# Kernel tuning notes

Hardware: AMD Instinct MI355X
Metric: run time of the kernel (lower is better)

Reference implementation:

```python
import jax, jax.numpy as jnp
import numpy as np

B, T, C, H = 8, 1024, 768, 12
HD = C // H  # 64


def setup_inputs() -> dict:
    key = jax.random.key(0)
    ks = jax.random.split(key, 9)
    s = 0.02
    x = jax.random.normal(ks[0], (B, T, C), dtype=jnp.float32)
    mask = jnp.tril(jnp.ones((T, T), dtype=bool))[None, None, :, :]  # causal [1,1,T,T]
    wq = jax.random.normal(ks[1], (C, C), dtype=jnp.float32) * s
    wk = jax.random.normal(ks[2], (C, C), dtype=jnp.float32) * s
    wv = jax.random.normal(ks[3], (C, C), dtype=jnp.float32) * s
    wo = jax.random.normal(ks[4], (C, C), dtype=jnp.float32) * s
    bq = jnp.zeros((C,), dtype=jnp.float32)
    bk = jnp.zeros((C,), dtype=jnp.float32)
    bv = jnp.zeros((C,), dtype=jnp.float32)
    bo = jnp.zeros((C,), dtype=jnp.float32)
    return {"x": x, "mask": mask, "wq": wq, "bq": bq, "wk": wk, "bk": bk,
            "wv": wv, "bv": bv, "wo": wo, "bo": bo}


def reference(x, mask, wq, bq, wk, bk, wv, bv, wo, bo):
    Bx, Tx, Cx = x.shape
    # QKV projections (flax Dense: y = x @ W + b)
    q = (x @ wq + bq).reshape(Bx, Tx, H, HD).transpose(0, 2, 1, 3)  # [B,H,T,hd]
    k = (x @ wk + bk).reshape(Bx, Tx, H, HD).transpose(0, 2, 1, 3)
    v = (x @ wv + bv).reshape(Bx, Tx, H, HD).transpose(0, 2, 1, 3)
    attn = jnp.einsum('bhtd,bhsd->bhts', q, k) / jnp.sqrt(jnp.float32(HD))
    attn = jnp.where(mask, attn, jnp.float32(-1e9))
    attn = jax.nn.softmax(attn, axis=-1)
    out = jnp.einsum('bhts,bhsd->bhtd', attn, v)  # [B,H,T,hd]
    out = out.transpose(0, 2, 1, 3).reshape(Bx, Tx, Cx)
    return out @ wo + bo
```

## Files before the change

kernel.cpp:

```cpp
#include <hip/hip_runtime.h>
#include <hip/hip_bf16.h>

typedef __bf16 bf16_t;
typedef __bf16 bf16x8 __attribute__((ext_vector_type(8)));
typedef float f32x4 __attribute__((ext_vector_type(4)));

#define NB 8
#define NT 1024
#define NC 768
#define NH 12
#define NHD 64

__device__ __forceinline__ f32x4 mfma16(bf16x8 a, bf16x8 b, f32x4 c) {
  return __builtin_amdgcn_mfma_f32_16x16x32_bf16(a, b, c, 0, 0, 0);
}

__device__ __forceinline__ void gld_lds16(const void* g, void* l) {
  __builtin_amdgcn_global_load_lds((const __attribute__((address_space(1))) void*)g,
                                   (__attribute__((address_space(3))) void*)l, 16, 0, 0);
}

__global__ void cvt_x(const float* __restrict__ in, bf16_t* __restrict__ out, int n4) {
  int i = blockIdx.x * blockDim.x + threadIdx.x;
  if (i >= n4) return;
  float4 v = ((const float4*)in)[i];
  bf16_t o[4] = {(bf16_t)v.x, (bf16_t)v.y, (bf16_t)v.z, (bf16_t)v.w};
  *(uint2*)(out + i * 4) = *(uint2*)o;
}

__global__ void transpose_w(const float* __restrict__ wq, const float* __restrict__ wk,
                            const float* __restrict__ wv, const float* __restrict__ wo,
                            bf16_t* __restrict__ wqkvT, bf16_t* __restrict__ woT) {
  __shared__ float tile[32][33];
  const int m = blockIdx.z;
  const float* in = (m == 0) ? wq : (m == 1) ? wk : (m == 2) ? wv : wo;
  bf16_t* out = (m == 3) ? woT : (wqkvT + m * NC * NC);
  const int tx = threadIdx.x & 31, ty = threadIdx.x >> 5;
  const int x = blockIdx.x * 32 + tx;
  const int y0 = blockIdx.y * 32;
#pragma unroll
  for (int i = 0; i < 32; i += 8)
    tile[ty + i][tx] = in[(size_t)(y0 + ty + i) * NC + x];
  __syncthreads();
  const int ox = y0 + tx;
  const int oy0 = blockIdx.x * 32;
#pragma unroll
  for (int i = 0; i < 32; i += 8)
    out[(size_t)(oy0 + ty + i) * NC + ox] = (bf16_t)tile[tx][ty + i];
}

template <int MODE>
__global__ __launch_bounds__(256) void gemm128(
    const bf16_t* __restrict__ A, const bf16_t* __restrict__ BT, int K,
    const float* __restrict__ b0, const float* __restrict__ b1,
    const float* __restrict__ b2, float* __restrict__ outF,
    bf16_t* __restrict__ out0, bf16_t* __restrict__ out1,
    bf16_t* __restrict__ out2) {
  __shared__ __align__(16) bf16_t lA[128 * 32];
  __shared__ __align__(16) bf16_t lB[128 * 32];
  const int tid = threadIdx.x;
  const int lane = tid & 63, wave = tid >> 6;
  const int quad = lane >> 4, l16 = lane & 15;
  const int bm = blockIdx.x * 128, bn = blockIdx.y * 128;
  const int wr = wave >> 1, wc = wave & 1;

  const int ra = tid >> 2;
  const int cc = tid & 3;
  const int kca = cc ^ ((ra >> 1) & 3);

  f32x4 acc[4][4] = {};
  char* lAb = (char*)lA;
  char* lBb = (char*)lB;

  for (int k0 = 0; k0 < K; k0 += 32) {
    __syncthreads();
    gld_lds16(A + (size_t)(bm + ra) * K + k0 + kca * 8, lAb + wave * 1024);
    gld_lds16(A + (size_t)(bm + 64 + ra) * K + k0 + kca * 8, lAb + 4096 + wave * 1024);
    gld_lds16(BT + (size_t)(bn + ra) * K + k0 + kca * 8, lBb + wave * 1024);
    gld_lds16(BT + (size_t)(bn + 64 + ra) * K + k0 + kca * 8, lBb + 4096 + wave * 1024);
    __syncthreads();

    bf16x8 af[4], bfr[4];
#pragma unroll
    for (int i = 0; i < 4; i++) {
      int row = wr * 64 + i * 16 + l16;
      int ch = quad ^ ((row >> 1) & 3);
      af[i] = *(const bf16x8*)(lAb + row * 64 + ch * 16);
    }
#pragma unroll
    for (int j = 0; j < 4; j++) {
      int row = wc * 64 + j * 16 + l16;
      int ch = quad ^ ((row >> 1) & 3);
      bfr[j] = *(const bf16x8*)(lBb + row * 64 + ch * 16);
    }
#pragma unroll
    for (int i = 0; i < 4; i++)
#pragma unroll
      for (int j = 0; j < 4; j++)
        acc[i][j] = mfma16(af[i], bfr[j], acc[i][j]);
  }

  if (MODE == 0) {
#pragma unroll
    for (int j = 0; j < 4; j++) {
      int n = bn + wc * 64 + j * 16 + l16;
      float bias = b0[n];
#pragma unroll
      for (int i = 0; i < 4; i++) {
        int m0 = bm + wr * 64 + i * 16 + quad * 4;
#pragma unroll
        for (int r = 0; r < 4; r++)
          outF[(size_t)(m0 + r) * NC + n] = acc[i][j][r] + bias;
      }
    }
  } else {
#pragma unroll
    for (int j = 0; j < 4; j++) {
      int n = bn + wc * 64 + j * 16 + l16;
      int sel = n / 768;
      int nl = n - sel * 768;
      int h = nl >> 6, d = nl & 63;
      const float* bp = (sel == 0) ? b0 : (sel == 1) ? b1 : b2;
      bf16_t* dst = (sel == 0) ? out0 : (sel == 1) ? out1 : out2;
      float bias = bp[nl];
#pragma unroll
      for (int i = 0; i < 4; i++) {
        int m0 = bm + wr * 64 + i * 16 + quad * 4;
#pragma unroll
        for (int r = 0; r < 4; r++) {
          int m = m0 + r;
          int bb = m >> 10, t = m & 1023;
          float v = acc[i][j][r] + bias;
          if (sel < 2)
            dst[((size_t)(bb * NH + h) * NT + t) * NHD + d] = (bf16_t)v;
          else
            dst[((size_t)(bb * NH + h) * NHD + d) * NT + t] = (bf16_t)v;
        }
      }
    }
  }
}

__global__ __launch_bounds__(256) void attn_fwd(
    const bf16_t* __restrict__ Q, const bf16_t* __restrict__ Kt,
    const bf16_t* __restrict__ VT, bf16_t* __restrict__ AO) {
  __shared__ __align__(16) bf16_t lK[64 * 72];
  __shared__ __align__(16) bf16_t lV[64 * 72];
  __shared__ __align__(16) bf16_t lP[8][16 * 72];
  const int tid = threadIdx.x, lane = tid & 63, wave = tid >> 6;
  const int quad = lane >> 4, l16 = lane & 15;
  const int bx = blockIdx.x;
  const int bh = blockIdx.y;
  const int b = bh / NH, h = bh - b * NH;
  const int qtA = bx, qtB = 15 - bx;
  const int jmax = qtB;

  const size_t qbase = (size_t)bh * NT;
  const size_t qoffA = (qbase + qtA * 64 + wave * 16 + l16) * NHD;
  const size_t qoffB = (qbase + qtB * 64 + wave * 16 + l16) * NHD;
  const bf16x8 aqA0 = *(const bf16x8*)(Q + qoffA + quad * 8);
  const bf16x8 aqA1 = *(const bf16x8*)(Q + qoffA + 32 + quad * 8);
  const bf16x8 aqB0 = *(const bf16x8*)(Q + qoffB + quad * 8);
  const bf16x8 aqB1 = *(const bf16x8*)(Q + qoffB + 32 + quad * 8);

  f32x4 mA = {-1e30f, -1e30f, -1e30f, -1e30f}, mB = mA;
  f32x4 lA_ = {0.f, 0.f, 0.f, 0.f}, lB_ = lA_;
  f32x4 OfA[4] = {}, OfB[4] = {};

  const int r0 = tid >> 3, p0 = tid & 7;
  const bf16_t* Kg0 = Kt + qbase * NHD;
  const bf16_t* Vg0 = VT + (size_t)bh * 64 * NT;

  uint4 gk0 = *(const uint4*)(Kg0 + (size_t)r0 * 64 + p0 * 8);
  uint4 gk1 = *(const uint4*)(Kg0 + (size_t)(r0 + 32) * 64 + p0 * 8);
  uint4 gv0 = *(const uint4*)(Vg0 + (size_t)r0 * NT + p0 * 8);
  uint4 gv1 = *(const uint4*)(Vg0 + (size_t)(r0 + 32) * NT + p0 * 8);

  bf16_t* lPA = lP[wave * 2 + 0];
  bf16_t* lPB = lP[wave * 2 + 1];
  const int sb = quad ^ (l16 >> 2);

  for (int j = 0; j <= jmax; ++j) {
    __syncthreads();
    *(uint4*)(lK + r0 * 72 + p0 * 8) = gk0;
    *(uint4*)(lK + (r0 + 32) * 72 + p0 * 8) = gk1;
    *(uint4*)(lV + r0 * 72 + p0 * 8) = gv0;
    *(uint4*)(lV + (r0 + 32) * 72 + p0 * 8) = gv1;
    __syncthreads();
    if (j < jmax) {
      const bf16_t* Kg = Kg0 + (size_t)(j + 1) * 64 * NHD;
      const bf16_t* Vg = Vg0 + (j + 1) * 64;
      gk0 = *(const uint4*)(Kg + (size_t)r0 * 64 + p0 * 8);
      gk1 = *(const uint4*)(Kg + (size_t)(r0 + 32) * 64 + p0 * 8);
      gv0 = *(const uint4*)(Vg + (size_t)r0 * NT + p0 * 8);
      gv1 = *(const uint4*)(Vg + (size_t)(r0 + 32) * NT + p0 * 8);
    }
    const bool actA = (j <= qtA);

#pragma unroll
    for (int g = 0; g < 2; g++) {
      if (g == 0 && !actA) continue;
      const bf16x8 q0 = g ? aqB0 : aqA0;
      const bf16x8 q1 = g ? aqB1 : aqA1;
      f32x4* Of = g ? OfB : OfA;
      f32x4& mrun = g ? mB : mA;
      f32x4& lrun = g ? lB_ : lA_;
      const bool diag = g ? (j == qtB) : (j == qtA);

      f32x4 s[4] = {};
#pragma unroll
      for (int nn = 0; nn < 4; nn++) {
        int row = nn * 16 + l16;
        bf16x8 k0 = *(const bf16x8*)(lK + row * 72 + quad * 8);
        bf16x8 k1 = *(const bf16x8*)(lK + row * 72 + 32 + quad * 8);
        s[nn] = mfma16(q0, k0, s[nn]);
        s[nn] = mfma16(q1, k1, s[nn]);
      }
#pragma unroll
      for (int nn = 0; nn < 4; nn++) s[nn] *= 0.125f;

      if (diag) {
#pragma unroll
        for (int nn = 0; nn < 4; nn++) {
          int key = nn * 16 + l16;
#pragma unroll
          for (int r = 0; r < 4; r++) {
            int qrow = wave * 16 + quad * 4 + r;
            if (key > qrow) s[nn][r] = -1e30f;
          }
        }
      }

      f32x4 mx = s[0];
#pragma unroll
      for (int nn = 1; nn < 4; nn++)
#pragma unroll
        for (int r = 0; r < 4; r++) mx[r] = fmaxf(mx[r], s[nn][r]);
#pragma unroll
      for (int off = 8; off >= 1; off >>= 1)
#pragma unroll
        for (int r = 0; r < 4; r++) mx[r] = fmaxf(mx[r], __shfl_xor(mx[r], off, 64));

      f32x4 mnew, alpha;
#pragma unroll
      for (int r = 0; r < 4; r++) {
        mnew[r] = fmaxf(mrun[r], mx[r]);
        alpha[r] = __expf(mrun[r] - mnew[r]);
        mrun[r] = mnew[r];
      }
      f32x4 rs = {0.f, 0.f, 0.f, 0.f};
#pragma unroll
      for (int nn = 0; nn < 4; nn++)
#pragma unroll
        for (int r = 0; r < 4; r++) {
          float pv = __expf(s[nn][r] - mnew[r]);
          s[nn][r] = pv;
          rs[r] += pv;
        }
#pragma unroll
      for (int off = 8; off >= 1; off >>= 1)
#pragma unroll
        for (int r = 0; r < 4; r++) rs[r] += __shfl_xor(rs[r], off, 64);
#pragma unroll
      for (int r = 0; r < 4; r++) lrun[r] = lrun[r] * alpha[r] + rs[r];
#pragma unroll
      for (int dd = 0; dd < 4; dd++)
#pragma unroll
        for (int r = 0; r < 4; r++) Of[dd][r] *= alpha[r];

      bf16_t* lPw = g ? lPB : lPA;
#pragma unroll
      for (int nn = 0; nn < 4; nn++)
#pragma unroll
        for (int r = 0; r < 4; r++)
          lPw[(quad * 4 + r) * 72 + ((nn * 16 + l16) ^ (quad * 8))] = (bf16_t)s[nn][r];
    }
    __syncthreads();

#pragma unroll
    for (int g = 0; g < 2; g++) {
      if (g == 0 && !actA) continue;
      f32x4* Of = g ? OfB : OfA;
      bf16_t* lPw = g ? lPB : lPA;
      const bf16x8 ap0 = *(const bf16x8*)(lPw + l16 * 72 + sb * 8);
      const bf16x8 ap1 = *(const bf16x8*)(lPw + l16 * 72 + (sb + 4) * 8);
#pragma unroll
      for (int dd = 0; dd < 4; dd++) {
        int row = dd * 16 + l16;
        bf16x8 v0 = *(const bf16x8*)(lV + row * 72 + quad * 8);
        bf16x8 v1 = *(const bf16x8*)(lV + row * 72 + 32 + quad * 8);
        Of[dd] = mfma16(ap0, v0, Of[dd]);
        Of[dd] = mfma16(ap1, v1, Of[dd]);
      }
    }
  }

#pragma unroll
  for (int g = 0; g < 2; g++) {
    f32x4* Of = g ? OfB : OfA;
    f32x4& lrun = g ? lB_ : lA_;
    const int qt = g ? qtB : qtA;
    f32x4 inv;
#pragma unroll
    for (int r = 0; r < 4; r++) inv[r] = 1.0f / lrun[r];
    const int tq = qt * 64 + wave * 16 + quad * 4;
#pragma unroll
    for (int dd = 0; dd < 4; dd++) {
      int col = h * 64 + dd * 16 + l16;
#pragma unroll
      for (int r = 0; r < 4; r++)
        AO[((size_t)b * NT + tq + r) * NC + col] = (bf16_t)(Of[dd][r] * inv[r]);
    }
  }
}

extern "C" void kernel_launch(void* const* d_in, const int* in_sizes, int n_in,
                              void* d_out, int out_size, void* d_ws, size_t ws_size,
                              hipStream_t stream) {
  const float* x = (const float*)d_in[0];
  const float* wq = (const float*)d_in[2];
  const float* bq = (const float*)d_in[3];
  const float* wk = (const float*)d_in[4];
  const float* bk = (const float*)d_in[5];
  const float* wv = (const float*)d_in[6];
  const float* bv = (const float*)d_in[7];
  const float* wo = (const float*)d_in[8];
  const float* bo = (const float*)d_in[9];

  float* outF = (float*)d_out;
  bf16_t* Qb = (bf16_t*)d_out;
  bf16_t* ws = (bf16_t*)d_ws;
  bf16_t* xb = ws;
  bf16_t* wqkvT = xb + (size_t)NB * NT * NC;
  bf16_t* woT = wqkvT + (size_t)2304 * 768;
  bf16_t* Kb = woT + (size_t)768 * 768;
  bf16_t* VTb = Kb + (size_t)NB * NH * NT * NHD;
  bf16_t* AO = VTb + (size_t)NB * NH * NT * NHD;

  const int n4 = NB * NT * NC / 4;
  cvt_x<<<(n4 + 255) / 256, 256, 0, stream>>>(x, xb, n4);
  transpose_w<<<dim3(24, 24, 4), 256, 0, stream>>>(wq, wk, wv, wo, wqkvT, woT);
  gemm128<1><<<dim3(64, 18), 256, 0, stream>>>(xb, wqkvT, NC, bq, bk, bv,
                                               nullptr, Qb, Kb, VTb);
  attn_fwd<<<dim3(8, 96), 256, 0, stream>>>(Qb, Kb, VTb, AO);
  gemm128<0><<<dim3(64, 6), 256, 0, stream>>>(AO, woT, NC, bo, nullptr, nullptr,
                                              outF, nullptr, nullptr, nullptr);
}
```

Before: 241.4 us.

## Transpose V in a separate kernel, fold softmax scale into Q, retile output GEMM

The QKV GEMM now writes V in the same row-major head layout as Q and K, which replaces the strided transposed stores in its epilogue. A new LDS-tiled kernel then produces the transposed V layout the attention kernel expects. The 1/sqrt(d) scale is applied to Q in the projection epilogue, so the per-tile multiply in attention goes away. In attention, a block-wide barrier before the P·V step becomes a per-wave LDS waitcnt, since each wave reads only its own P buffer. The output projection uses 64-row tiles, giving twice as many blocks. The costs are an extra kernel launch and an extra pass over V, and the barrier removal relies on per-wave ownership of the P buffers.

New measurement: 233.8 us. -3.1%, faster.

```diff
diff --git a/kernel.cpp b/kernel.cpp
--- a/kernel.cpp
+++ b/kernel.cpp
@@ -49,65 +49,85 @@
     out[(size_t)(oy0 + ty + i) * NC + ox] = (bf16_t)tile[tx][ty + i];
 }
 
-template <int MODE>
-__global__ __launch_bounds__(256) void gemm128(
+__global__ void transpose_v(const bf16_t* __restrict__ V, bf16_t* __restrict__ VT) {
+  __shared__ bf16_t tile[32][33];
+  const int bh = blockIdx.z;
+  const int x0 = blockIdx.x * 32;
+  const int y0 = blockIdx.y * 32;
+  const int tx = threadIdx.x & 31, ty = threadIdx.x >> 5;
+  const bf16_t* in = V + (size_t)bh * NT * NHD;
+  bf16_t* out = VT + (size_t)bh * NHD * NT;
+#pragma unroll
+  for (int i = 0; i < 32; i += 8)
+    tile[ty + i][tx] = in[(size_t)(y0 + ty + i) * NHD + x0 + tx];
+  __syncthreads();
+#pragma unroll
+  for (int i = 0; i < 32; i += 8)
+    out[(size_t)(x0 + ty + i) * NT + y0 + tx] = tile[tx][ty + i];
+}
+
+template <int MODE, int BM>
+__global__ __launch_bounds__(256) void gemm_t(
     const bf16_t* __restrict__ A, const bf16_t* __restrict__ BT, int K,
     const float* __restrict__ b0, const float* __restrict__ b1,
     const float* __restrict__ b2, float* __restrict__ outF,
     bf16_t* __restrict__ out0, bf16_t* __restrict__ out1,
     bf16_t* __restrict__ out2) {
-  __shared__ __align__(16) bf16_t lA[128 * 32];
+  constexpr int NJ = (BM == 128) ? 4 : 2;
+  __shared__ __align__(16) bf16_t lA[BM * 32];
   __shared__ __align__(16) bf16_t lB[128 * 32];
   const int tid = threadIdx.x;
   const int lane = tid & 63, wave = tid >> 6;
   const int quad = lane >> 4, l16 = lane & 15;
-  const int bm = blockIdx.x * 128, bn = blockIdx.y * 128;
-  const int wr = wave >> 1, wc = wave & 1;
+  const int bm = blockIdx.x * BM, bn = blockIdx.y * 128;
+  const int wm = (BM == 128) ? (wave >> 1) * 64 : 0;
+  const int wn = (BM == 128) ? (wave & 1) * 64 : wave * 32;
 
   const int ra = tid >> 2;
   const int cc = tid & 3;
   const int kca = cc ^ ((ra >> 1) & 3);
 
-  f32x4 acc[4][4] = {};
+  f32x4 acc[4][NJ] = {};
   char* lAb = (char*)lA;
   char* lBb = (char*)lB;
 
   for (int k0 = 0; k0 < K; k0 += 32) {
     __syncthreads();
     gld_lds16(A + (size_t)(bm + ra) * K + k0 + kca * 8, lAb + wave * 1024);
-    gld_lds16(A + (size_t)(bm + 64 + ra) * K + k0 + kca * 8, lAb + 4096 + wave * 1024);
+    if (BM == 128)
+      gld_lds16(A + (size_t)(bm + 64 + ra) * K + k0 + kca * 8, lAb + 4096 + wave * 1024);
     gld_lds16(BT + (size_t)(bn + ra) * K + k0 + kca * 8, lBb + wave * 1024);
     gld_lds16(BT + (size_t)(bn + 64 + ra) * K + k0 + kca * 8, lBb + 4096 + wave * 1024);
     __syncthreads();
 
-    bf16x8 af[4], bfr[4];
+    bf16x8 af[4], bfr[NJ];
 #pragma unroll
     for (int i = 0; i < 4; i++) {
-      int row = wr * 64 + i * 16 + l16;
+      int row = wm + i * 16 + l16;
       int ch = quad ^ ((row >> 1) & 3);
       af[i] = *(const bf16x8*)(lAb + row * 64 + ch * 16);
     }
 #pragma unroll
-    for (int j = 0; j < 4; j++) {
-      int row = wc * 64 + j * 16 + l16;
+    for (int j = 0; j < NJ; j++) {
+      int row = wn + j * 16 + l16;
       int ch = quad ^ ((row >> 1) & 3);
       bfr[j] = *(const bf16x8*)(lBb + row * 64 + ch * 16);
     }
 #pragma unroll
     for (int i = 0; i < 4; i++)
 #pragma unroll
-      for (int j = 0; j < 4; j++)
+      for (int j = 0; j < NJ; j++)
         acc[i][j] = mfma16(af[i], bfr[j], acc[i][j]);
   }
 
   if (MODE == 0) {
 #pragma unroll
-    for (int j = 0; j < 4; j++) {
-      int n = bn + wc * 64 + j * 16 + l16;
+    for (int j = 0; j < NJ; j++) {
+      int n = bn + wn + j * 16 + l16;
       float bias = b0[n];
 #pragma unroll
       for (int i = 0; i < 4; i++) {
-        int m0 = bm + wr * 64 + i * 16 + quad * 4;
+        int m0 = bm + wm + i * 16 + quad * 4;
 #pragma unroll
         for (int r = 0; r < 4; r++)
           outF[(size_t)(m0 + r) * NC + n] = acc[i][j][r] + bias;
@@ -115,26 +135,24 @@
     }
   } else {
 #pragma unroll
-    for (int j = 0; j < 4; j++) {
-      int n = bn + wc * 64 + j * 16 + l16;
+    for (int j = 0; j < NJ; j++) {
+      int n = bn + wn + j * 16 + l16;
       int sel = n / 768;
       int nl = n - sel * 768;
       int h = nl >> 6, d = nl & 63;
       const float* bp = (sel == 0) ? b0 : (sel == 1) ? b1 : b2;
       bf16_t* dst = (sel == 0) ? out0 : (sel == 1) ? out1 : out2;
       float bias = bp[nl];
+      float scl = (sel == 0) ? 0.125f : 1.0f;
 #pragma unroll
       for (int i = 0; i < 4; i++) {
-        int m0 = bm + wr * 64 + i * 16 + quad * 4;
+        int m0 = bm + wm + i * 16 + quad * 4;
 #pragma unroll
         for (int r = 0; r < 4; r++) {
           int m = m0 + r;
           int bb = m >> 10, t = m & 1023;
-          float v = acc[i][j][r] + bias;
-          if (sel < 2)
-            dst[((size_t)(bb * NH + h) * NT + t) * NHD + d] = (bf16_t)v;
-          else
-            dst[((size_t)(bb * NH + h) * NHD + d) * NT + t] = (bf16_t)v;
+          dst[((size_t)(bb * NH + h) * NT + t) * NHD + d] =
+              (bf16_t)((acc[i][j][r] + bias) * scl);
         }
       }
     }
@@ -216,8 +234,6 @@
         s[nn] = mfma16(q0, k0, s[nn]);
         s[nn] = mfma16(q1, k1, s[nn]);
       }
-#pragma unroll
-      for (int nn = 0; nn < 4; nn++) s[nn] *= 0.125f;
 
       if (diag) {
 #pragma unroll
@@ -275,7 +291,7 @@
         for (int r = 0; r < 4; r++)
           lPw[(quad * 4 + r) * 72 + ((nn * 16 + l16) ^ (quad * 8))] = (bf16_t)s[nn][r];
     }
-    __syncthreads();
+    asm volatile("s_waitcnt lgkmcnt(0)" ::: "memory");
 
 #pragma unroll
     for (int g = 0; g < 2; g++) {
@@ -329,6 +345,7 @@
 
   float* outF = (float*)d_out;
   bf16_t* Qb = (bf16_t*)d_out;
+  bf16_t* Vb = Qb + (size_t)NB * NH * NT * NHD;
   bf16_t* ws = (bf16_t*)d_ws;
   bf16_t* xb = ws;
   bf16_t* wqkvT = xb + (size_t)NB * NT * NC;
@@ -340,9 +357,10 @@
   const int n4 = NB * NT * NC / 4;
   cvt_x<<<(n4 + 255) / 256, 256, 0, stream>>>(x, xb, n4);
   transpose_w<<<dim3(24, 24, 4), 256, 0, stream>>>(wq, wk, wv, wo, wqkvT, woT);
-  gemm128<1><<<dim3(64, 18), 256, 0, stream>>>(xb, wqkvT, NC, bq, bk, bv,
-                                               nullptr, Qb, Kb, VTb);
+  gemm_t<1, 128><<<dim3(64, 18), 256, 0, stream>>>(xb, wqkvT, NC, bq, bk, bv,
+                                                   nullptr, Qb, Kb, Vb);
+  transpose_v<<<dim3(2, 32, 96), 256, 0, stream>>>(Vb, VTb);
   attn_fwd<<<dim3(8, 96), 256, 0, stream>>>(Qb, Kb, VTb, AO);
-  gemm128<0><<<dim3(64, 6), 256, 0, stream>>>(AO, woT, NC, bo, nullptr, nullptr,
-                                              outF, nullptr, nullptr, nullptr);
-}
+  gemm_t<0, 64><<<dim3(128, 6), 256, 0, stream>>>(AO, woT, NC, bo, nullptr, nullptr,
+                                                  outF, nullptr, nullptr, nullptr);
+}
```
